# Optimization experiments

Hardware: AMD Instinct MI355X
Metric: run time of the kernel (lower is better)

The kernel has to match this reference:

```python
import jax, jax.numpy as jnp
import numpy as np

INPUT_DIM = 64
RESERVOIR_DIM = 2048
OUTPUT_DIM = 64
SPECTRAL_RADIUS = 0.9
LEAK_RATE = 0.3
SPARSITY = 0.9
INPUT_SCALING = 1.0
NOISE_LEVEL = 0.01
T = 4096


def setup_inputs() -> dict:
    key = jax.random.key(0)
    k_u, k_n = jax.random.split(key)
    u = jax.random.normal(k_u, (T, INPUT_DIM), dtype=jnp.float32)
    noise = jax.random.normal(k_n, (T, RESERVOIR_DIM), dtype=jnp.float32)

    # Reservoir weights, built exactly like the torch __init__ (fixed, untrained).
    rng = np.random.default_rng(0)
    W_in = (rng.standard_normal((RESERVOIR_DIM, INPUT_DIM)) * INPUT_SCALING).astype(np.float32)
    W = (rng.uniform(0.0, 1.0, (RESERVOIR_DIM, RESERVOIR_DIM)) * 2.0 - 1.0).astype(np.float32)
    mask = rng.uniform(0.0, 1.0, (RESERVOIR_DIM, RESERVOIR_DIM)) > SPARSITY
    W = W * mask.astype(np.float32)
    sr = np.max(np.abs(np.linalg.eigvals(W)))  # spectral radius normalization
    W = (W * (SPECTRAL_RADIUS / sr)).astype(np.float32)

    # nn.Linear(reservoir_dim, output_dim) init: U(-1/sqrt(N), 1/sqrt(N))
    bound = 1.0 / np.sqrt(RESERVOIR_DIM)
    readout_w = rng.uniform(-bound, bound, (OUTPUT_DIM, RESERVOIR_DIM)).astype(np.float32)
    readout_b = rng.uniform(-bound, bound, (OUTPUT_DIM,)).astype(np.float32)

    return {
        "u": u,
        "noise": noise,
        "W_in": jnp.asarray(W_in),
        "W": jnp.asarray(W),
        "readout_w": jnp.asarray(readout_w),
        "readout_b": jnp.asarray(readout_b),
    }


def reference(u, noise, W_in, W, readout_w, readout_b):
    # Leaky-integrated ESN recurrence, state reset to zeros (reset_state=True).
    input_terms = u @ W_in.T + noise * NOISE_LEVEL  # [T, N], precompute input GEMM

    def step(state, it):
        new_state = jnp.tanh(it + W @ state)
        state = (1.0 - LEAK_RATE) * state + LEAK_RATE * new_state
        return state, state

    init = jnp.zeros((RESERVOIR_DIM,), dtype=u.dtype)
    _, states = jax.lax.scan(step, init, input_terms)  # states: [T, N]
    return states @ readout_w.T + readout_b  # [T, output_dim]
```

## Files before the change

### kernel.cpp

```cpp
#include <hip/hip_runtime.h>

#define T_STEPS 4096
#define N_RES   2048
#define N_IN    64
#define N_OUT   64
#define LEAK    0.3f
#define NOISE_S 0.01f

typedef unsigned int uint32x4 __attribute__((ext_vector_type(4)));

__global__ __launch_bounds__(256) void input_terms_kernel(
    const float* __restrict__ u, const float* __restrict__ noise,
    const float* __restrict__ W_in, float* __restrict__ it) {
  const int t = blockIdx.x;
  const int tid = threadIdx.x;
  __shared__ float su[N_IN];
  if (tid < N_IN) su[tid] = u[(size_t)t * N_IN + tid];
  __syncthreads();
  #pragma unroll
  for (int k = 0; k < N_RES / 256; ++k) {
    const int n = tid + 256 * k;
    const float4* wr = reinterpret_cast<const float4*>(W_in + (size_t)n * N_IN);
    float acc = 0.f;
    #pragma unroll
    for (int j = 0; j < N_IN / 4; ++j) {
      float4 w4 = wr[j];
      acc = fmaf(w4.x, su[4 * j + 0], acc);
      acc = fmaf(w4.y, su[4 * j + 1], acc);
      acc = fmaf(w4.z, su[4 * j + 2], acc);
      acc = fmaf(w4.w, su[4 * j + 3], acc);
    }
    it[(size_t)t * N_RES + n] = acc + NOISE_S * noise[(size_t)t * N_RES + n];
  }
}

__global__ __launch_bounds__(256, 1) void reservoir_kernel(
    const float* __restrict__ W, float* __restrict__ it,
    unsigned int* sbuf) {
  const int wg = blockIdx.x;
  const int tid = threadIdx.x;
  const int wave = tid >> 6;
  const int lane = tid & 63;
  const int R = wg * 8;
  const int r0 = R + wave * 2;

  __shared__ float Wl[8 * N_RES];
  __shared__ float ls[N_RES];
  __shared__ float stg[8];

  {
    const float4* Wg = reinterpret_cast<const float4*>(W + (size_t)R * N_RES);
    float4* Wd = reinterpret_cast<float4*>(Wl);
    #pragma unroll
    for (int k = 0; k < 16; ++k) Wd[tid + 256 * k] = Wg[tid + 256 * k];
  }
  __syncthreads();

  const float4* S4 = reinterpret_cast<const float4*>(ls);
  const float4* W0 = reinterpret_cast<const float4*>(Wl + (size_t)(2 * wave) * N_RES);
  const float4* W1 = reinterpret_cast<const float4*>(Wl + (size_t)(2 * wave + 1) * N_RES);
  uint32x4* lsv = reinterpret_cast<uint32x4*>(ls);

  for (unsigned int t = 0; t < T_STEPS; ++t) {
    const unsigned int* srb = sbuf + (t & 1) * N_RES;
    unsigned int* swb = sbuf + ((t + 1) & 1) * N_RES;
    const unsigned int tag = t & 3u;

    float itv = 0.f;
    if (lane < 2) itv = it[(size_t)t * N_RES + r0 + lane];

    {
      const uint32x4* pa = reinterpret_cast<const uint32x4*>(srb) + tid;
      const uint32x4* pb = pa + 256;
      unsigned int need = 3u;
      for (;;) {
        uint32x4 va, vb;
        if (need == 3u) {
          asm volatile(
              "global_load_dwordx4 %0, %2, off sc0 sc1\n\t"
              "global_load_dwordx4 %1, %3, off sc0 sc1\n\t"
              "s_waitcnt vmcnt(0)"
              : "=&v"(va), "=&v"(vb)
              : "v"(pa), "v"(pb)
              : "memory");
          if ((((va[0] ^ tag) | (va[1] ^ tag) | (va[2] ^ tag) | (va[3] ^ tag)) & 3u) == 0u) {
            lsv[tid] = va;
            need &= ~1u;
          }
          if ((((vb[0] ^ tag) | (vb[1] ^ tag) | (vb[2] ^ tag) | (vb[3] ^ tag)) & 3u) == 0u) {
            lsv[256 + tid] = vb;
            need &= ~2u;
          }
        } else if (need == 1u) {
          asm volatile(
              "global_load_dwordx4 %0, %1, off sc0 sc1\n\t"
              "s_waitcnt vmcnt(0)"
              : "=&v"(va) : "v"(pa) : "memory");
          if ((((va[0] ^ tag) | (va[1] ^ tag) | (va[2] ^ tag) | (va[3] ^ tag)) & 3u) == 0u) {
            lsv[tid] = va;
            need = 0u;
          }
        } else {
          asm volatile(
              "global_load_dwordx4 %0, %1, off sc0 sc1\n\t"
              "s_waitcnt vmcnt(0)"
              : "=&v"(vb) : "v"(pb) : "memory");
          if ((((vb[0] ^ tag) | (vb[1] ^ tag) | (vb[2] ^ tag) | (vb[3] ^ tag)) & 3u) == 0u) {
            lsv[256 + tid] = vb;
            need = 0u;
          }
        }
        if (!need) break;
        __builtin_amdgcn_s_sleep(1);
      }
    }
    __syncthreads();

    float a0 = 0.f, a1 = 0.f;
    #pragma unroll
    for (int j = 0; j < 8; ++j) {
      const float4 s4 = S4[lane + 64 * j];
      const float4 x0 = W0[lane + 64 * j];
      const float4 x1 = W1[lane + 64 * j];
      a0 = fmaf(x0.x, s4.x, a0); a0 = fmaf(x0.y, s4.y, a0);
      a0 = fmaf(x0.z, s4.z, a0); a0 = fmaf(x0.w, s4.w, a0);
      a1 = fmaf(x1.x, s4.x, a1); a1 = fmaf(x1.y, s4.y, a1);
      a1 = fmaf(x1.z, s4.z, a1); a1 = fmaf(x1.w, s4.w, a1);
    }
    #pragma unroll
    for (int off = 32; off > 0; off >>= 1) {
      a0 += __shfl_xor(a0, off);
      a1 += __shfl_xor(a1, off);
    }

    if (lane < 2) {
      const float a = lane ? a1 : a0;
      const float h = tanhf(itv + a);
      const float sold = ls[r0 + lane];
      const float snew = (1.0f - LEAK) * sold + LEAK * h;
      stg[wave * 2 + lane] = snew;
      it[(size_t)t * N_RES + r0 + lane] = snew;
    }
    __syncthreads();

    if (tid < 2) {
      const unsigned int tg = (t + 1) & 3u;
      uint32x4 pk;
      #pragma unroll
      for (int j = 0; j < 4; ++j)
        pk[j] = (__float_as_uint(stg[4 * tid + j]) & ~3u) | tg;
      uint32x4* dst = reinterpret_cast<uint32x4*>(swb) + wg * 2 + tid;
      asm volatile("global_store_dwordx4 %0, %1, off sc0 sc1"
                   :: "v"(dst), "v"(pk) : "memory");
    }
  }
}

__global__ __launch_bounds__(256) void readout_kernel(
    const float* __restrict__ states, const float* __restrict__ rw,
    const float* __restrict__ rb, float* __restrict__ out) {
  const int t = blockIdx.x;
  const int tid = threadIdx.x;
  const int o = tid & 63;
  const int q = tid >> 6;
  __shared__ float ss[N_RES];
  #pragma unroll
  for (int k = 0; k < N_RES / 256; ++k)
    ss[tid + 256 * k] = states[(size_t)t * N_RES + tid + 256 * k];
  __syncthreads();

  const float4* r4 = reinterpret_cast<const float4*>(rw + (size_t)o * N_RES + q * 512);
  float acc = 0.f;
  #pragma unroll 8
  for (int j = 0; j < 128; ++j) {
    float4 w4 = r4[j];
    const int base = q * 512 + 4 * j;
    acc = fmaf(w4.x, ss[base + 0], acc);
    acc = fmaf(w4.y, ss[base + 1], acc);
    acc = fmaf(w4.z, ss[base + 2], acc);
    acc = fmaf(w4.w, ss[base + 3], acc);
  }
  __shared__ float red[256];
  red[tid] = acc;
  __syncthreads();
  if (tid < 64) {
    float v = red[tid] + red[tid + 64] + red[tid + 128] + red[tid + 192];
    out[(size_t)t * N_OUT + tid] = v + rb[tid];
  }
}

extern "C" void kernel_launch(void* const* d_in, const int* in_sizes, int n_in,
                              void* d_out, int out_size, void* d_ws, size_t ws_size,
                              hipStream_t stream) {
  const float* u     = (const float*)d_in[0];
  const float* noise = (const float*)d_in[1];
  const float* W_in  = (const float*)d_in[2];
  const float* W     = (const float*)d_in[3];
  const float* rw    = (const float*)d_in[4];
  const float* rb    = (const float*)d_in[5];
  float* out = (float*)d_out;

  float* it = (float*)d_ws;
  unsigned int* sbuf =
      (unsigned int*)((char*)d_ws + (size_t)T_STEPS * N_RES * sizeof(float));

  hipMemsetAsync(sbuf, 0, 2 * N_RES * sizeof(unsigned int), stream);

  input_terms_kernel<<<T_STEPS, 256, 0, stream>>>(u, noise, W_in, it);

  void* args[] = {(void*)&W, (void*)&it, (void*)&sbuf};
  hipLaunchCooperativeKernel((void*)reservoir_kernel, dim3(256), dim3(256),
                             args, 0, stream);

  readout_kernel<<<T_STEPS, 256, 0, stream>>>(it, rw, rb, out);
}
```

Before: 11.54 ms.

## Halve reservoir workgroups, double-buffer LDS state, drop per-step barrier

The recurrence kernel now runs on 128 workgroups, each holding 16 rows of W in LDS (128KB), with four rows per wave instead of two. The LDS state vector is double-buffered, and each wave publishes its own four new state values directly through a shuffle and a single tagged store, which removes the staging array and one __syncthreads per step. Fewer producers mean fewer tagged chunks to poll per step and less cross-workgroup sync latency, in exchange for twice the per-step dot-product work on each CU and a larger LDS footprint.

```diff
diff --git a/kernel.cpp b/kernel.cpp
--- a/kernel.cpp
+++ b/kernel.cpp
@@ -6,6 +6,10 @@
 #define N_OUT   64
 #define LEAK    0.3f
 #define NOISE_S 0.01f
+
+#define NWG     128
+#define RPW     16
+#define RPWAVE  4
 
 typedef unsigned int uint32x4 __attribute__((ext_vector_type(4)));
 
@@ -41,37 +45,111 @@
   const int tid = threadIdx.x;
   const int wave = tid >> 6;
   const int lane = tid & 63;
-  const int R = wg * 8;
-  const int r0 = R + wave * 2;
-
-  __shared__ float Wl[8 * N_RES];
-  __shared__ float ls[N_RES];
-  __shared__ float stg[8];
+  const int R = wg * RPW;
+  const int r0 = R + wave * RPWAVE;
+
+  __shared__ float Wl[RPW * N_RES];
+  __shared__ float ls[2][N_RES];
 
   {
     const float4* Wg = reinterpret_cast<const float4*>(W + (size_t)R * N_RES);
     float4* Wd = reinterpret_cast<float4*>(Wl);
     #pragma unroll
-    for (int k = 0; k < 16; ++k) Wd[tid + 256 * k] = Wg[tid + 256 * k];
-  }
-  __syncthreads();
-
-  const float4* S4 = reinterpret_cast<const float4*>(ls);
-  const float4* W0 = reinterpret_cast<const float4*>(Wl + (size_t)(2 * wave) * N_RES);
-  const float4* W1 = reinterpret_cast<const float4*>(Wl + (size_t)(2 * wave + 1) * N_RES);
-  uint32x4* lsv = reinterpret_cast<uint32x4*>(ls);
+    for (int k = 0; k < RPW * N_RES / 4 / 256; ++k)
+      Wd[tid + 256 * k] = Wg[tid + 256 * k];
+  }
+
+  float itv = 0.f;
+  if (lane < RPWAVE) itv = it[r0 + lane];
+
+  {
+    const uint32x4* pa = reinterpret_cast<const uint32x4*>(sbuf) + tid;
+    const uint32x4* pb = pa + 256;
+    uint32x4* dsta = reinterpret_cast<uint32x4*>(&ls[0][0]) + tid;
+    uint32x4* dstb = dsta + 256;
+    unsigned int need = 3u;
+    while (need) {
+      uint32x4 va, vb;
+      asm volatile(
+          "global_load_dwordx4 %0, %2, off sc0 sc1\n\t"
+          "global_load_dwordx4 %1, %3, off sc0 sc1\n\t"
+          "s_waitcnt vmcnt(0)"
+          : "=&v"(va), "=&v"(vb) : "v"(pa), "v"(pb) : "memory");
+      if ((need & 1u) &&
+          (((va[0] | va[1] | va[2] | va[3]) & 3u) == 0u)) { *dsta = va; need &= ~1u; }
+      if ((need & 2u) &&
+          (((vb[0] | vb[1] | vb[2] | vb[3]) & 3u) == 0u)) { *dstb = vb; need &= ~2u; }
+      if (need) __builtin_amdgcn_s_sleep(1);
+    }
+  }
+  __syncthreads();
 
   for (unsigned int t = 0; t < T_STEPS; ++t) {
-    const unsigned int* srb = sbuf + (t & 1) * N_RES;
+    const float* cur = ls[t & 1];
+    float* nxt = ls[(t + 1) & 1];
     unsigned int* swb = sbuf + ((t + 1) & 1) * N_RES;
-    const unsigned int tag = t & 3u;
-
-    float itv = 0.f;
-    if (lane < 2) itv = it[(size_t)t * N_RES + r0 + lane];
+
+    const float4* S4 = reinterpret_cast<const float4*>(cur);
+    const float4* W0 = reinterpret_cast<const float4*>(Wl + (size_t)(RPWAVE * wave + 0) * N_RES);
+    const float4* W1 = reinterpret_cast<const float4*>(Wl + (size_t)(RPWAVE * wave + 1) * N_RES);
+    const float4* W2 = reinterpret_cast<const float4*>(Wl + (size_t)(RPWAVE * wave + 2) * N_RES);
+    const float4* W3 = reinterpret_cast<const float4*>(Wl + (size_t)(RPWAVE * wave + 3) * N_RES);
+    float a0 = 0.f, a1 = 0.f, a2 = 0.f, a3 = 0.f;
+    #pragma unroll
+    for (int j = 0; j < N_RES / 4 / 64; ++j) {
+      const float4 s4 = S4[lane + 64 * j];
+      const float4 x0 = W0[lane + 64 * j];
+      const float4 x1 = W1[lane + 64 * j];
+      const float4 x2 = W2[lane + 64 * j];
+      const float4 x3 = W3[lane + 64 * j];
+      a0 = fmaf(x0.x, s4.x, a0); a0 = fmaf(x0.y, s4.y, a0);
+      a0 = fmaf(x0.z, s4.z, a0); a0 = fmaf(x0.w, s4.w, a0);
+      a1 = fmaf(x1.x, s4.x, a1); a1 = fmaf(x1.y, s4.y, a1);
+      a1 = fmaf(x1.z, s4.z, a1); a1 = fmaf(x1.w, s4.w, a1);
+      a2 = fmaf(x2.x, s4.x, a2); a2 = fmaf(x2.y, s4.y, a2);
+      a2 = fmaf(x2.z, s4.z, a2); a2 = fmaf(x2.w, s4.w, a2);
+      a3 = fmaf(x3.x, s4.x, a3); a3 = fmaf(x3.y, s4.y, a3);
+      a3 = fmaf(x3.z, s4.z, a3); a3 = fmaf(x3.w, s4.w, a3);
+    }
+    #pragma unroll
+    for (int off = 32; off > 0; off >>= 1) {
+      a0 += __shfl_xor(a0, off);
+      a1 += __shfl_xor(a1, off);
+      a2 += __shfl_xor(a2, off);
+      a3 += __shfl_xor(a3, off);
+    }
+
+    float snew = 0.f;
+    if (lane < RPWAVE) {
+      const float a = (lane == 0) ? a0 : (lane == 1) ? a1 : (lane == 2) ? a2 : a3;
+      const float h = tanhf(itv + a);
+      const float sold = cur[r0 + lane];
+      snew = (1.0f - LEAK) * sold + LEAK * h;
+      it[(size_t)t * N_RES + r0 + lane] = snew;
+    }
 
     {
-      const uint32x4* pa = reinterpret_cast<const uint32x4*>(srb) + tid;
+      const unsigned int tg = (t + 1) & 3u;
+      uint32x4 pk;
+      pk[0] = (__float_as_uint(__shfl(snew, 0)) & ~3u) | tg;
+      pk[1] = (__float_as_uint(__shfl(snew, 1)) & ~3u) | tg;
+      pk[2] = (__float_as_uint(__shfl(snew, 2)) & ~3u) | tg;
+      pk[3] = (__float_as_uint(__shfl(snew, 3)) & ~3u) | tg;
+      if (lane == 0) {
+        uint32x4* dst = reinterpret_cast<uint32x4*>(swb) + (r0 >> 2);
+        asm volatile("global_store_dwordx4 %0, %1, off sc0 sc1"
+                     :: "v"(dst), "v"(pk) : "memory");
+      }
+    }
+
+    if (t + 1 < T_STEPS) {
+      if (lane < RPWAVE) itv = it[(size_t)(t + 1) * N_RES + r0 + lane];
+
+      const unsigned int tag = (t + 1) & 3u;
+      const uint32x4* pa = reinterpret_cast<const uint32x4*>(swb) + tid;
       const uint32x4* pb = pa + 256;
+      uint32x4* dsta = reinterpret_cast<uint32x4*>(nxt) + tid;
+      uint32x4* dstb = dsta + 256;
       unsigned int need = 3u;
       for (;;) {
         uint32x4 va, vb;
@@ -80,16 +158,12 @@
               "global_load_dwordx4 %0, %2, off sc0 sc1\n\t"
               "global_load_dwordx4 %1, %3, off sc0 sc1\n\t"
               "s_waitcnt vmcnt(0)"
-              : "=&v"(va), "=&v"(vb)
-              : "v"(pa), "v"(pb)
-              : "memory");
+              : "=&v"(va), "=&v"(vb) : "v"(pa), "v"(pb) : "memory");
           if ((((va[0] ^ tag) | (va[1] ^ tag) | (va[2] ^ tag) | (va[3] ^ tag)) & 3u) == 0u) {
-            lsv[tid] = va;
-            need &= ~1u;
+            *dsta = va; need &= ~1u;
           }
           if ((((vb[0] ^ tag) | (vb[1] ^ tag) | (vb[2] ^ tag) | (vb[3] ^ tag)) & 3u) == 0u) {
-            lsv[256 + tid] = vb;
-            need &= ~2u;
+            *dstb = vb; need &= ~2u;
           }
         } else if (need == 1u) {
           asm volatile(
@@ -97,8 +171,7 @@
               "s_waitcnt vmcnt(0)"
               : "=&v"(va) : "v"(pa) : "memory");
           if ((((va[0] ^ tag) | (va[1] ^ tag) | (va[2] ^ tag) | (va[3] ^ tag)) & 3u) == 0u) {
-            lsv[tid] = va;
-            need = 0u;
+            *dsta = va; need = 0u;
           }
         } else {
           asm volatile(
@@ -106,8 +179,7 @@
               "s_waitcnt vmcnt(0)"
               : "=&v"(vb) : "v"(pb) : "memory");
           if ((((vb[0] ^ tag) | (vb[1] ^ tag) | (vb[2] ^ tag) | (vb[3] ^ tag)) & 3u) == 0u) {
-            lsv[256 + tid] = vb;
-            need = 0u;
+            *dstb = vb; need = 0u;
           }
         }
         if (!need) break;
@@ -115,44 +187,6 @@
       }
     }
     __syncthreads();
-
-    float a0 = 0.f, a1 = 0.f;
-    #pragma unroll
-    for (int j = 0; j < 8; ++j) {
-      const float4 s4 = S4[lane + 64 * j];
-      const float4 x0 = W0[lane + 64 * j];
-      const float4 x1 = W1[lane + 64 * j];
-      a0 = fmaf(x0.x, s4.x, a0); a0 = fmaf(x0.y, s4.y, a0);
-      a0 = fmaf(x0.z, s4.z, a0); a0 = fmaf(x0.w, s4.w, a0);
-      a1 = fmaf(x1.x, s4.x, a1); a1 = fmaf(x1.y, s4.y, a1);
-      a1 = fmaf(x1.z, s4.z, a1); a1 = fmaf(x1.w, s4.w, a1);
-    }
-    #pragma unroll
-    for (int off = 32; off > 0; off >>= 1) {
-      a0 += __shfl_xor(a0, off);
-      a1 += __shfl_xor(a1, off);
-    }
-
-    if (lane < 2) {
-      const float a = lane ? a1 : a0;
-      const float h = tanhf(itv + a);
-      const float sold = ls[r0 + lane];
-      const float snew = (1.0f - LEAK) * sold + LEAK * h;
-      stg[wave * 2 + lane] = snew;
-      it[(size_t)t * N_RES + r0 + lane] = snew;
-    }
-    __syncthreads();
-
-    if (tid < 2) {
-      const unsigned int tg = (t + 1) & 3u;
-      uint32x4 pk;
-      #pragma unroll
-      for (int j = 0; j < 4; ++j)
-        pk[j] = (__float_as_uint(stg[4 * tid + j]) & ~3u) | tg;
-      uint32x4* dst = reinterpret_cast<uint32x4*>(swb) + wg * 2 + tid;
-      asm volatile("global_store_dwordx4 %0, %1, off sc0 sc1"
-                   :: "v"(dst), "v"(pk) : "memory");
-    }
   }
 }
 
@@ -209,7 +243,7 @@
   input_terms_kernel<<<T_STEPS, 256, 0, stream>>>(u, noise, W_in, it);
 
   void* args[] = {(void*)&W, (void*)&it, (void*)&sbuf};
-  hipLaunchCooperativeKernel((void*)reservoir_kernel, dim3(256), dim3(256),
+  hipLaunchCooperativeKernel((void*)reservoir_kernel, dim3(NWG), dim3(256),
                              args, 0, stream);
 
   readout_kernel<<<T_STEPS, 256, 0, stream>>>(it, rw, rb, out);
```

After: 13.63 ms. 1.18x slower.
